# Performance work log

Hardware: AMD Instinct MI355X
Metric: run time of the kernel (lower is better)

## Reference

```python
import math
import jax, jax.numpy as jnp
import numpy as np

B, T, C, H = 1, 2048, 1024, 16


def _rope(q, k):
    # q, k: (B, H, T, D); interleaved RoPE exactly as the torch helper
    D = q.shape[-1]
    pos = jnp.arange(q.shape[2], dtype=jnp.float32)[:, None]           # (T, 1)
    div = jnp.exp(jnp.arange(0, D, 2, dtype=jnp.float32) * (-math.log(10000.0) / D))
    ang = pos * div                                                     # (T, D/2)
    sin = jnp.repeat(jnp.sin(ang), 2, axis=-1)                          # [s0,s0,s1,s1,...]
    cos = jnp.repeat(jnp.cos(ang), 2, axis=-1)

    def rot(x):
        x_alt = jnp.stack([-x[..., 1::2], x[..., ::2]], axis=-1).reshape(x.shape)
        return x * cos + x_alt * sin

    return rot(q), rot(k)


def setup_inputs() -> dict:
    key = jax.random.key(0)
    ks = jax.random.split(key, 5)
    s = 1.0 / math.sqrt(C)
    return {
        "x": jax.random.normal(ks[0], (B, T, C), dtype=jnp.float32),
        "Wq": jax.random.normal(ks[1], (C, C), dtype=jnp.float32) * s,
        "bq": jnp.zeros((C,), dtype=jnp.float32),
        "Wk": jax.random.normal(ks[2], (C, C), dtype=jnp.float32) * s,
        "bk": jnp.zeros((C,), dtype=jnp.float32),
        "Wv": jax.random.normal(ks[3], (C, C), dtype=jnp.float32) * s,
        "bv": jnp.zeros((C,), dtype=jnp.float32),
        "Wp": jax.random.normal(ks[4], (C, C), dtype=jnp.float32) * s,
        "bp": jnp.zeros((C,), dtype=jnp.float32),
    }


def reference(x, Wq, bq, Wk, bk, Wv, bv, Wp, bp):
    b, t, c = x.shape
    d = c // H
    # QKV projections -> (B, H, T, D)
    def split_heads(y):
        return y.reshape(b, t, H, d).transpose(0, 2, 1, 3)

    q = split_heads(x @ Wq + bq)
    k = split_heads(x @ Wk + bk)
    v = split_heads(x @ Wv + bv)
    q, k = _rope(q, k)

    scale = 1.0 / math.sqrt(d)
    att = jnp.einsum("bhqd,bhkd->bhqk", q, k) * scale                   # (B,H,T,T)
    causal = jnp.tril(jnp.ones((t, t), dtype=bool))                     # (T,T)
    att = jnp.where(causal[None, None], att, -jnp.inf)
    att = jax.nn.softmax(att, axis=-1)
    attn_save = att
    # dropout p=0 (eval) -> identity
    y = jnp.einsum("bhqk,bhkd->bhqd", att, v)                           # (B,H,T,D)
    y = y.transpose(0, 2, 1, 3).reshape(b, t, c)
    y = y @ Wp + bp
    return y, attn_save
```

## Files before the change

kernel.cpp:

```cpp
#include <hip/hip_runtime.h>

typedef unsigned short ushort_t;
typedef __bf16 bf16x8 __attribute__((ext_vector_type(8)));
typedef float f32x4 __attribute__((ext_vector_type(4)));

#define T_DIM 2048
#define C_DIM 1024
#define H_NUM 16
#define D_DIM 64

__device__ __forceinline__ ushort_t f2bf(float f){
  unsigned v = __float_as_uint(f);
  return (ushort_t)((v + 0x7fffu + ((v >> 16) & 1u)) >> 16);
}
__device__ __forceinline__ float bf2f(ushort_t u){
  return __uint_as_float(((unsigned)u) << 16);
}

typedef __attribute__((address_space(1))) const unsigned int* gas1_t;
typedef __attribute__((address_space(3))) unsigned int* las3_t;

__device__ __forceinline__ void gload_lds16(const void* g, void* l){
  __builtin_amdgcn_global_load_lds((gas1_t)g, (las3_t)l, 16, 0, 0);
}

__global__ __launch_bounds__(256) void prep_kernel(
    const float* __restrict__ x, ushort_t* __restrict__ xb,
    const float* __restrict__ w0, const float* __restrict__ w1,
    const float* __restrict__ w2, const float* __restrict__ w3,
    ushort_t* __restrict__ t0, ushort_t* __restrict__ t1,
    ushort_t* __restrict__ t2, ushort_t* __restrict__ t3)
{
  __shared__ float tl[64][65];
  const int bid = blockIdx.x;
  const int tid = threadIdx.x;
  if (bid >= 1024){
    int i = ((bid - 1024) * 256 + tid) * 4;
    float4 v = *reinterpret_cast<const float4*>(x + i);
    ushort4 o;
    o.x = f2bf(v.x); o.y = f2bf(v.y); o.z = f2bf(v.z); o.w = f2bf(v.w);
    *reinterpret_cast<ushort4*>(xb + i) = o;
    return;
  }
  const int which = bid >> 8;
  const float* W = which==0 ? w0 : which==1 ? w1 : which==2 ? w2 : w3;
  ushort_t* WT   = which==0 ? t0 : which==1 ? t1 : which==2 ? t2 : t3;
  const int tile = bid & 255;
  const int k0 = (tile & 15) * 64;
  const int n0 = (tile >> 4) * 64;
#pragma unroll
  for (int i = 0; i < 16; ++i){
    int idx = tid + i * 256;
    int r = idx >> 6, c = idx & 63;
    tl[r][c] = W[(k0 + r) * C_DIM + n0 + c];
  }
  __syncthreads();
#pragma unroll
  for (int i = 0; i < 16; ++i){
    int idx = tid + i * 256;
    int r = idx >> 6, c = idx & 63;
    WT[(n0 + r) * C_DIM + k0 + c] = f2bf(tl[c][r]);
  }
}

template<int MODE>
__global__ __launch_bounds__(256) void gemm_kernel(
    const ushort_t* __restrict__ A,
    const ushort_t* __restrict__ bt0, const ushort_t* __restrict__ bt1, const ushort_t* __restrict__ bt2,
    const float* __restrict__ bias0, const float* __restrict__ bias1, const float* __restrict__ bias2,
    ushort_t* __restrict__ o0, ushort_t* __restrict__ o1, ushort_t* __restrict__ o2,
    float* __restrict__ fo)
{
  __shared__ __align__(16) ushort_t Alds[64 * 32];
  __shared__ __align__(16) ushort_t Blds[128 * 32];
  const int tid = threadIdx.x;
  const int l15 = tid & 15, g = (tid & 63) >> 4;
  const int w = tid >> 6, wr = w >> 1, wc = w & 1;
  const int m0 = blockIdx.x * 64;
  int byy = blockIdx.y;
  int sel = 0;
  const ushort_t* BT; const float* bias; ushort_t* outp;
  if (MODE == 0){
    sel = byy >> 3; byy &= 7;
    BT   = sel==0 ? bt0 : (sel==1 ? bt1 : bt2);
    bias = sel==0 ? bias0 : (sel==1 ? bias1 : bias2);
    outp = sel==0 ? o0 : (sel==1 ? o1 : o2);
  } else { BT = bt0; bias = bias0; outp = o0; }
  const int n0 = byy * 128;

  const int c0 = tid, c1 = tid + 256;
  const ushort_t* Asrc  = A + (m0 + (c0 >> 2)) * C_DIM + (c0 & 3) * 8;
  const ushort_t* Bsrc0 = BT + (n0 + (c0 >> 2)) * C_DIM + (c0 & 3) * 8;
  const ushort_t* Bsrc1 = BT + (n0 + (c1 >> 2)) * C_DIM + (c1 & 3) * 8;

  f32x4 acc[2][4] = {};

  for (int kt = 0; kt < 32; ++kt){
    const int ko = kt * 32;
    gload_lds16(Asrc + ko, &Alds[c0 * 8]);
    gload_lds16(Bsrc0 + ko, &Blds[c0 * 8]);
    gload_lds16(Bsrc1 + ko, &Blds[c1 * 8]);
    __syncthreads();
    bf16x8 af[2], bfr[4];
#pragma unroll
    for (int i = 0; i < 2; ++i)
      af[i] = *reinterpret_cast<const bf16x8*>(&Alds[(wr * 32 + i * 16 + l15) * 32 + g * 8]);
#pragma unroll
    for (int j = 0; j < 4; ++j)
      bfr[j] = *reinterpret_cast<const bf16x8*>(&Blds[(wc * 64 + j * 16 + l15) * 32 + g * 8]);
#pragma unroll
    for (int i = 0; i < 2; ++i)
#pragma unroll
      for (int j = 0; j < 4; ++j)
        acc[i][j] = __builtin_amdgcn_mfma_f32_16x16x32_bf16(af[i], bfr[j], acc[i][j], 0, 0, 0);
    __syncthreads();
  }

  float bvv[4];
#pragma unroll
  for (int j = 0; j < 4; ++j) bvv[j] = bias[n0 + wc * 64 + j * 16 + l15];

  if (MODE == 1){
#pragma unroll
    for (int i = 0; i < 2; ++i)
#pragma unroll
      for (int j = 0; j < 4; ++j)
#pragma unroll
        for (int e = 0; e < 4; ++e){
          int t = m0 + wr * 32 + i * 16 + g * 4 + e;
          int c = n0 + wc * 64 + j * 16 + l15;
          fo[t * C_DIM + c] = acc[i][j][e] + bvv[j];
        }
    return;
  }

  if (sel == 2){
#pragma unroll
    for (int i = 0; i < 2; ++i){
#pragma unroll
      for (int j = 0; j < 4; ++j){
        int c = n0 + wc * 64 + j * 16 + l15;
        int hh = c >> 6, d = c & 63;
        int t0e = m0 + wr * 32 + i * 16 + g * 4;
        ushort4 o;
        o.x = f2bf(acc[i][j][0] + bvv[j]);
        o.y = f2bf(acc[i][j][1] + bvv[j]);
        o.z = f2bf(acc[i][j][2] + bvv[j]);
        o.w = f2bf(acc[i][j][3] + bvv[j]);
        *reinterpret_cast<ushort4*>(outp + (size_t)(hh * D_DIM + d) * T_DIM + t0e) = o;
      }
    }
  } else {
#pragma unroll
    for (int i = 0; i < 2; ++i){
#pragma unroll
      for (int j = 0; j < 4; ++j){
#pragma unroll
        for (int e = 0; e < 4; ++e){
          int t = m0 + wr * 32 + i * 16 + g * 4 + e;
          int c = n0 + wc * 64 + j * 16 + l15;
          int hh = c >> 6, d = c & 63;
          outp[((size_t)(hh * T_DIM) + t) * D_DIM + d] = f2bf(acc[i][j][e] + bvv[j]);
        }
      }
    }
  }
}

__global__ void rope_kernel(ushort_t* __restrict__ Qb, ushort_t* __restrict__ Kb){
  int gid = blockIdx.x * 256 + threadIdx.x;
  int which = gid >> 20;
  int r = gid & ((1 << 20) - 1);
  int i = r & 31;
  int t = (r >> 5) & 2047;
  int hh = r >> 16;
  ushort_t* P = which ? Kb : Qb;
  unsigned* p = reinterpret_cast<unsigned*>(P + ((hh * T_DIM) + t) * D_DIM + 2 * i);
  unsigned pv = *p;
  float x0 = bf2f((ushort_t)(pv & 0xffffu));
  float x1 = bf2f((ushort_t)(pv >> 16));
  float ang = (float)t * __expf((float)i * -0.2878231366242558f);
  float sn, cs;
  __sincosf(ang, &sn, &cs);
  float y0 = x0 * cs - x1 * sn;
  float y1 = x1 * cs + x0 * sn;
  *p = (unsigned)f2bf(y0) | (((unsigned)f2bf(y1)) << 16);
}

__global__ __launch_bounds__(256) void attn_kernel(
    const ushort_t* __restrict__ Qb, const ushort_t* __restrict__ Kb,
    const ushort_t* __restrict__ Vt, float* __restrict__ att, ushort_t* __restrict__ ya)
{
  __shared__ __align__(16) ushort_t Plds[2][64 * 72];
  __shared__ float m_sh[64], l_sh[64];

  const int tid = threadIdx.x;
  const int l15 = tid & 15, g = (tid & 63) >> 4;
  const int w = tid >> 6, wr = w >> 1, wc = w & 1;
  const int lin = (int)blockIdx.x;
  const int h = 2 * (lin & 7) + ((lin >> 3) & 1);
  const int qi = (T_DIM / 64 - 1) - (lin >> 4);
  const int q0 = qi * 64;
  const int nkt = qi + 1;

  const ushort_t* Qh = Qb + h * T_DIM * D_DIM;
  const ushort_t* Kh = Kb + h * T_DIM * D_DIM;
  const ushort_t* Vh = Vt + h * D_DIM * T_DIM;
  float* atth = att + (size_t)h * T_DIM * T_DIM;

  const f32x4 fz = {0.f, 0.f, 0.f, 0.f};
  const float scale = 0.125f;

  const int qloc = w * 16 + l15;
  const int qglob = q0 + qloc;
  bf16x8 qT[2];
#pragma unroll
  for (int ks = 0; ks < 2; ++ks)
    qT[ks] = *reinterpret_cast<const bf16x8*>(Qh + qglob * D_DIM + ks * 32 + g * 8);

  float m1 = -1e30f, l1 = 0.f;

  for (int kt = 0; kt < nkt; ++kt){
    f32x4 sc[4];
    sc[0] = fz; sc[1] = fz; sc[2] = fz; sc[3] = fz;
#pragma unroll
    for (int mblk = 0; mblk < 4; ++mblk){
#pragma unroll
      for (int ks = 0; ks < 2; ++ks){
        bf16x8 kfT = *reinterpret_cast<const bf16x8*>(
            Kh + (kt * 64 + mblk * 16 + l15) * D_DIM + ks * 32 + g * 8);
        sc[mblk] = __builtin_amdgcn_mfma_f32_16x16x32_bf16(kfT, qT[ks], sc[mblk], 0, 0, 0);
      }
    }
    const bool diag = (kt == qi);
    const int kbase = kt * 64 + g * 4;
    float sv[16];
    float mx = -1e30f;
#pragma unroll
    for (int mblk = 0; mblk < 4; ++mblk){
#pragma unroll
      for (int j = 0; j < 4; ++j){
        float s = sc[mblk][j] * scale;
        if (diag && (kbase + mblk * 16 + j) > qglob) s = -1e30f;
        sv[mblk * 4 + j] = s;
        mx = fmaxf(mx, s);
      }
    }
    mx = fmaxf(mx, __shfl_xor(mx, 16));
    mx = fmaxf(mx, __shfl_xor(mx, 32));
    float mn = fmaxf(m1, mx);
    float ps = 0.f;
#pragma unroll
    for (int i = 0; i < 16; ++i) ps += __expf(sv[i] - mn);
    ps += __shfl_xor(ps, 16);
    ps += __shfl_xor(ps, 32);
    l1 = l1 * __expf(m1 - mn) + ps;
    m1 = mn;
  }

  if ((tid & 48) == 0){ m_sh[qloc] = m1; l_sh[qloc] = l1; }
  __syncthreads();

  float Mrow[2][4], Li[2][4];
#pragma unroll
  for (int ms = 0; ms < 2; ++ms)
#pragma unroll
    for (int j = 0; j < 4; ++j){
      int row = wr * 32 + ms * 16 + g * 4 + j;
      Mrow[ms][j] = m_sh[row];
      Li[ms][j] = 1.0f / l_sh[row];
    }

  bf16x8 qf[2][2];
#pragma unroll
  for (int ms = 0; ms < 2; ++ms)
#pragma unroll
    for (int ks = 0; ks < 2; ++ks)
      qf[ms][ks] = *reinterpret_cast<const bf16x8*>(
          Qh + (q0 + wr * 32 + ms * 16 + l15) * D_DIM + ks * 32 + g * 8);

  f32x4 yac[2][2];
  yac[0][0] = fz; yac[0][1] = fz; yac[1][0] = fz; yac[1][1] = fz;

  int pb = 0;
  for (int kt = 0; kt < nkt; ++kt){
    ushort_t* Pb = &Plds[pb][0];
    bf16x8 kf[2][2];
#pragma unroll
    for (int ns = 0; ns < 2; ++ns)
#pragma unroll
      for (int ks = 0; ks < 2; ++ks)
        kf[ns][ks] = *reinterpret_cast<const bf16x8*>(
            Kh + (kt * 64 + wc * 32 + ns * 16 + l15) * D_DIM + ks * 32 + g * 8);

    f32x4 sac[2][2];
    sac[0][0] = fz; sac[0][1] = fz; sac[1][0] = fz; sac[1][1] = fz;
#pragma unroll
    for (int ms = 0; ms < 2; ++ms)
#pragma unroll
      for (int ns = 0; ns < 2; ++ns)
#pragma unroll
        for (int ks = 0; ks < 2; ++ks)
          sac[ms][ns] = __builtin_amdgcn_mfma_f32_16x16x32_bf16(qf[ms][ks], kf[ns][ks], sac[ms][ns], 0, 0, 0);

    const bool diag = (kt == qi);
#pragma unroll
    for (int ms = 0; ms < 2; ++ms)
#pragma unroll
      for (int ns = 0; ns < 2; ++ns)
#pragma unroll
        for (int j = 0; j < 4; ++j){
          float s = sac[ms][ns][j] * scale;
          int qq = wr * 32 + ms * 16 + g * 4 + j;
          int cc = wc * 32 + ns * 16 + l15;
          if (diag && cc > qq) s = -1e30f;
          float p = __expf(s - Mrow[ms][j]) * Li[ms][j];
          Pb[qq * 72 + cc] = f2bf(p);
        }
    __syncthreads();

    bf16x8 pf[2][2], vf[2][2];
#pragma unroll
    for (int ms = 0; ms < 2; ++ms)
#pragma unroll
      for (int kk = 0; kk < 2; ++kk)
        pf[ms][kk] = *reinterpret_cast<const bf16x8*>(
            &Pb[(wr * 32 + ms * 16 + l15) * 72 + kk * 32 + g * 8]);
#pragma unroll
    for (int nd = 0; nd < 2; ++nd)
#pragma unroll
      for (int kk = 0; kk < 2; ++kk)
        vf[nd][kk] = *reinterpret_cast<const bf16x8*>(
            Vh + (wc * 32 + nd * 16 + l15) * T_DIM + kt * 64 + kk * 32 + g * 8);
#pragma unroll
    for (int ms = 0; ms < 2; ++ms)
#pragma unroll
      for (int nd = 0; nd < 2; ++nd)
#pragma unroll
        for (int kk = 0; kk < 2; ++kk)
          yac[ms][nd] = __builtin_amdgcn_mfma_f32_16x16x32_bf16(pf[ms][kk], vf[nd][kk], yac[ms][nd], 0, 0, 0);

#pragma unroll
    for (int half = 0; half < 2; ++half){
      const int c = tid + half * 256;
      const int r = c >> 3, s = c & 7;
      union { int4 i4; ushort_t us[8]; } u;
      u.i4 = *reinterpret_cast<const int4*>(&Pb[r * 72 + s * 8]);
      f32x4 lo = { bf2f(u.us[0]), bf2f(u.us[1]), bf2f(u.us[2]), bf2f(u.us[3]) };
      f32x4 hi = { bf2f(u.us[4]), bf2f(u.us[5]), bf2f(u.us[6]), bf2f(u.us[7]) };
      float* dst = atth + (size_t)(q0 + r) * T_DIM + kt * 64 + s * 8;
      *reinterpret_cast<f32x4*>(dst)     = lo;
      *reinterpret_cast<f32x4*>(dst + 4) = hi;
    }
    pb ^= 1;
  }

  const int zc0 = nkt * 64;
  const int cpr = (T_DIM - zc0) >> 2;
  if (cpr > 0){
    const f32x4 z = {0.f, 0.f, 0.f, 0.f};
    for (int r = 0; r < 64; ++r){
      f32x4* dst = reinterpret_cast<f32x4*>(atth + (size_t)(q0 + r) * T_DIM + zc0);
      for (int i = tid; i < cpr; i += 256)
        dst[i] = z;
    }
  }

#pragma unroll
  for (int ms = 0; ms < 2; ++ms)
#pragma unroll
    for (int nd = 0; nd < 2; ++nd)
#pragma unroll
      for (int j = 0; j < 4; ++j){
        int t = q0 + wr * 32 + ms * 16 + g * 4 + j;
        int dcol = wc * 32 + nd * 16 + l15;
        ya[t * C_DIM + h * D_DIM + dcol] = f2bf(yac[ms][nd][j]);
      }
}

extern "C" void kernel_launch(void* const* d_in, const int* in_sizes, int n_in,
                              void* d_out, int out_size, void* d_ws, size_t ws_size,
                              hipStream_t stream)
{
  const float* x  = (const float*)d_in[0];
  const float* Wq = (const float*)d_in[1];
  const float* bq = (const float*)d_in[2];
  const float* Wk = (const float*)d_in[3];
  const float* bk = (const float*)d_in[4];
  const float* Wv = (const float*)d_in[5];
  const float* bv = (const float*)d_in[6];
  const float* Wp = (const float*)d_in[7];
  const float* bp = (const float*)d_in[8];
  float* out = (float*)d_out;
  char* ws = (char*)d_ws;

  ushort_t* xb  = (ushort_t*)(ws);
  ushort_t* wtq = (ushort_t*)(ws + (4u  << 20));
  ushort_t* wtk = (ushort_t*)(ws + (6u  << 20));
  ushort_t* wtv = (ushort_t*)(ws + (8u  << 20));
  ushort_t* wtp = (ushort_t*)(ws + (10u << 20));
  ushort_t* Qb  = (ushort_t*)(ws + (12u << 20));
  ushort_t* Kb  = (ushort_t*)(ws + (16u << 20));
  ushort_t* Vt  = (ushort_t*)(ws + (20u << 20));
  ushort_t* ya  = (ushort_t*)(ws + (24u << 20));

  hipLaunchKernelGGL(prep_kernel, dim3(3072), dim3(256), 0, stream,
                     x, xb, Wq, Wk, Wv, Wp, wtq, wtk, wtv, wtp);
  hipLaunchKernelGGL((gemm_kernel<0>), dim3(32, 24), dim3(256), 0, stream,
                     xb, wtq, wtk, wtv, bq, bk, bv, Qb, Kb, Vt, nullptr);
  hipLaunchKernelGGL(rope_kernel, dim3(8192), dim3(256), 0, stream, Qb, Kb);
  hipLaunchKernelGGL(attn_kernel, dim3(512), dim3(256), 0, stream,
                     Qb, Kb, Vt, out + 2097152, ya);
  hipLaunchKernelGGL((gemm_kernel<1>), dim3(32, 8), dim3(256), 0, stream,
                     ya, wtp, nullptr, nullptr, bp, nullptr, nullptr,
                     nullptr, nullptr, nullptr, out);
}
```

Before: 179.2 us.

## Split attention second pass across waves by key tiles with staged wide stores

Restructures the second attention pass so that each of the four waves processes a different key tile for the same 16-row query group, instead of splitting work in a 2x2 grid within one tile. Probabilities for up to 16 key tiles go into a wide LDS buffer, which is then written out to the attention matrix as a row-contiguous burst. Per-wave partial outputs are summed through LDS before the bf16 store. This removes the per-tile barrier and aims for longer contiguous writes to the large attention output. In exchange it adds a cross-wave reduction, reloads K and V fragments per row group, and leaves waves unevenly loaded on short causal rows.

```diff
diff --git a/kernel.cpp b/kernel.cpp
--- a/kernel.cpp
+++ b/kernel.cpp
@@ -8,6 +8,7 @@
 #define C_DIM 1024
 #define H_NUM 16
 #define D_DIM 64
+#define PWPAD 1032
 
 __device__ __forceinline__ ushort_t f2bf(float f){
   unsigned v = __float_as_uint(f);
@@ -191,12 +192,13 @@
     const ushort_t* __restrict__ Qb, const ushort_t* __restrict__ Kb,
     const ushort_t* __restrict__ Vt, float* __restrict__ att, ushort_t* __restrict__ ya)
 {
-  __shared__ __align__(16) ushort_t Plds[2][64 * 72];
+  __shared__ __align__(16) ushort_t Pw[16][PWPAD];
+  __shared__ __align__(16) float Osc[4][16][64];
   __shared__ float m_sh[64], l_sh[64];
 
   const int tid = threadIdx.x;
   const int l15 = tid & 15, g = (tid & 63) >> 4;
-  const int w = tid >> 6, wr = w >> 1, wc = w & 1;
+  const int w = tid >> 6;
   const int lin = (int)blockIdx.x;
   const int h = 2 * (lin & 7) + ((lin >> 3) & 1);
   const int qi = (T_DIM / 64 - 1) - (lin >> 4);
@@ -261,121 +263,112 @@
   if ((tid & 48) == 0){ m_sh[qloc] = m1; l_sh[qloc] = l1; }
   __syncthreads();
 
-  float Mrow[2][4], Li[2][4];
-#pragma unroll
-  for (int ms = 0; ms < 2; ++ms)
+  for (int rg = 0; rg < 4; ++rg){
+    bf16x8 qa[2];
+#pragma unroll
+    for (int ks = 0; ks < 2; ++ks)
+      qa[ks] = *reinterpret_cast<const bf16x8*>(
+          Qh + (q0 + rg * 16 + l15) * D_DIM + ks * 32 + g * 8);
+
+    float Mr[4], Lr[4];
 #pragma unroll
     for (int j = 0; j < 4; ++j){
-      int row = wr * 32 + ms * 16 + g * 4 + j;
-      Mrow[ms][j] = m_sh[row];
-      Li[ms][j] = 1.0f / l_sh[row];
-    }
-
-  bf16x8 qf[2][2];
-#pragma unroll
-  for (int ms = 0; ms < 2; ++ms)
-#pragma unroll
-    for (int ks = 0; ks < 2; ++ks)
-      qf[ms][ks] = *reinterpret_cast<const bf16x8*>(
-          Qh + (q0 + wr * 32 + ms * 16 + l15) * D_DIM + ks * 32 + g * 8);
-
-  f32x4 yac[2][2];
-  yac[0][0] = fz; yac[0][1] = fz; yac[1][0] = fz; yac[1][1] = fz;
-
-  int pb = 0;
-  for (int kt = 0; kt < nkt; ++kt){
-    ushort_t* Pb = &Plds[pb][0];
-    bf16x8 kf[2][2];
-#pragma unroll
-    for (int ns = 0; ns < 2; ++ns)
-#pragma unroll
-      for (int ks = 0; ks < 2; ++ks)
-        kf[ns][ks] = *reinterpret_cast<const bf16x8*>(
-            Kh + (kt * 64 + wc * 32 + ns * 16 + l15) * D_DIM + ks * 32 + g * 8);
-
-    f32x4 sac[2][2];
-    sac[0][0] = fz; sac[0][1] = fz; sac[1][0] = fz; sac[1][1] = fz;
-#pragma unroll
-    for (int ms = 0; ms < 2; ++ms)
-#pragma unroll
-      for (int ns = 0; ns < 2; ++ns)
-#pragma unroll
-        for (int ks = 0; ks < 2; ++ks)
-          sac[ms][ns] = __builtin_amdgcn_mfma_f32_16x16x32_bf16(qf[ms][ks], kf[ns][ks], sac[ms][ns], 0, 0, 0);
-
-    const bool diag = (kt == qi);
-#pragma unroll
-    for (int ms = 0; ms < 2; ++ms)
-#pragma unroll
-      for (int ns = 0; ns < 2; ++ns)
-#pragma unroll
-        for (int j = 0; j < 4; ++j){
-          float s = sac[ms][ns][j] * scale;
-          int qq = wr * 32 + ms * 16 + g * 4 + j;
-          int cc = wc * 32 + ns * 16 + l15;
-          if (diag && cc > qq) s = -1e30f;
-          float p = __expf(s - Mrow[ms][j]) * Li[ms][j];
-          Pb[qq * 72 + cc] = f2bf(p);
-        }
+      int row = rg * 16 + g * 4 + j;
+      Mr[j] = m_sh[row];
+      Lr[j] = 1.0f / l_sh[row];
+    }
+
+    f32x4 yac[4];
+    yac[0] = fz; yac[1] = fz; yac[2] = fz; yac[3] = fz;
+
+    const int nch = (nkt + 15) >> 4;
+    for (int ch = 0; ch < nch; ++ch){
+      const int ktbase = ch * 16;
+      const int ktend  = (ktbase + 16 < nkt) ? (ktbase + 16) : nkt;
+
+      for (int kt = ktbase + w; kt < ktend; kt += 4){
+        const int ktl = kt - ktbase;
+        f32x4 sac[4];
+        sac[0] = fz; sac[1] = fz; sac[2] = fz; sac[3] = fz;
+#pragma unroll
+        for (int ns = 0; ns < 4; ++ns){
+#pragma unroll
+          for (int ks = 0; ks < 2; ++ks){
+            bf16x8 kf = *reinterpret_cast<const bf16x8*>(
+                Kh + (kt * 64 + ns * 16 + l15) * D_DIM + ks * 32 + g * 8);
+            sac[ns] = __builtin_amdgcn_mfma_f32_16x16x32_bf16(qa[ks], kf, sac[ns], 0, 0, 0);
+          }
+        }
+        const bool diag = (kt == qi);
+#pragma unroll
+        for (int ns = 0; ns < 4; ++ns){
+#pragma unroll
+          for (int j = 0; j < 4; ++j){
+            float s = sac[ns][j] * scale;
+            int key = kt * 64 + ns * 16 + l15;
+            int qrow = q0 + rg * 16 + g * 4 + j;
+            if (diag && key > qrow) s = -1e30f;
+            float p = __expf(s - Mr[j]) * Lr[j];
+            Pw[g * 4 + j][ktl * 64 + ns * 16 + l15] = f2bf(p);
+          }
+        }
+#pragma unroll
+        for (int kk = 0; kk < 2; ++kk){
+          bf16x8 pf = *reinterpret_cast<const bf16x8*>(
+              &Pw[l15][ktl * 64 + kk * 32 + g * 8]);
+#pragma unroll
+          for (int nd = 0; nd < 4; ++nd){
+            bf16x8 vf = *reinterpret_cast<const bf16x8*>(
+                Vh + (nd * 16 + l15) * T_DIM + kt * 64 + kk * 32 + g * 8);
+            yac[nd] = __builtin_amdgcn_mfma_f32_16x16x32_bf16(pf, vf, yac[nd], 0, 0, 0);
+          }
+        }
+      }
+      __syncthreads();
+
+      const int wcols = (ktend - ktbase) * 64;
+      const int col = tid * 4;
+      if (col < wcols){
+#pragma unroll 4
+        for (int r = 0; r < 16; ++r){
+          ushort4 pv4 = *reinterpret_cast<const ushort4*>(&Pw[r][col]);
+          f32x4 o = { bf2f(pv4.x), bf2f(pv4.y), bf2f(pv4.z), bf2f(pv4.w) };
+          *reinterpret_cast<f32x4*>(
+              atth + (size_t)(q0 + rg * 16 + r) * T_DIM + ktbase * 64 + col) = o;
+        }
+      }
+      __syncthreads();
+    }
+
+    {
+      const int zc0 = nkt * 64;
+      for (int r = 0; r < 16; ++r){
+        float* rowp = atth + (size_t)(q0 + rg * 16 + r) * T_DIM;
+        for (int col = zc0 + tid * 4; col < T_DIM; col += 1024)
+          *reinterpret_cast<f32x4*>(rowp + col) = fz;
+      }
+    }
+
+#pragma unroll
+    for (int nd = 0; nd < 4; ++nd)
+#pragma unroll
+      for (int j = 0; j < 4; ++j)
+        Osc[w][g * 4 + j][nd * 16 + l15] = yac[nd][j];
     __syncthreads();
-
-    bf16x8 pf[2][2], vf[2][2];
-#pragma unroll
-    for (int ms = 0; ms < 2; ++ms)
-#pragma unroll
-      for (int kk = 0; kk < 2; ++kk)
-        pf[ms][kk] = *reinterpret_cast<const bf16x8*>(
-            &Pb[(wr * 32 + ms * 16 + l15) * 72 + kk * 32 + g * 8]);
-#pragma unroll
-    for (int nd = 0; nd < 2; ++nd)
-#pragma unroll
-      for (int kk = 0; kk < 2; ++kk)
-        vf[nd][kk] = *reinterpret_cast<const bf16x8*>(
-            Vh + (wc * 32 + nd * 16 + l15) * T_DIM + kt * 64 + kk * 32 + g * 8);
-#pragma unroll
-    for (int ms = 0; ms < 2; ++ms)
-#pragma unroll
-      for (int nd = 0; nd < 2; ++nd)
-#pragma unroll
-        for (int kk = 0; kk < 2; ++kk)
-          yac[ms][nd] = __builtin_amdgcn_mfma_f32_16x16x32_bf16(pf[ms][kk], vf[nd][kk], yac[ms][nd], 0, 0, 0);
-
-#pragma unroll
-    for (int half = 0; half < 2; ++half){
-      const int c = tid + half * 256;
-      const int r = c >> 3, s = c & 7;
-      union { int4 i4; ushort_t us[8]; } u;
-      u.i4 = *reinterpret_cast<const int4*>(&Pb[r * 72 + s * 8]);
-      f32x4 lo = { bf2f(u.us[0]), bf2f(u.us[1]), bf2f(u.us[2]), bf2f(u.us[3]) };
-      f32x4 hi = { bf2f(u.us[4]), bf2f(u.us[5]), bf2f(u.us[6]), bf2f(u.us[7]) };
-      float* dst = atth + (size_t)(q0 + r) * T_DIM + kt * 64 + s * 8;
-      *reinterpret_cast<f32x4*>(dst)     = lo;
-      *reinterpret_cast<f32x4*>(dst + 4) = hi;
-    }
-    pb ^= 1;
-  }
-
-  const int zc0 = nkt * 64;
-  const int cpr = (T_DIM - zc0) >> 2;
-  if (cpr > 0){
-    const f32x4 z = {0.f, 0.f, 0.f, 0.f};
-    for (int r = 0; r < 64; ++r){
-      f32x4* dst = reinterpret_cast<f32x4*>(atth + (size_t)(q0 + r) * T_DIM + zc0);
-      for (int i = tid; i < cpr; i += 256)
-        dst[i] = z;
-    }
-  }
-
-#pragma unroll
-  for (int ms = 0; ms < 2; ++ms)
-#pragma unroll
-    for (int nd = 0; nd < 2; ++nd)
-#pragma unroll
-      for (int j = 0; j < 4; ++j){
-        int t = q0 + wr * 32 + ms * 16 + g * 4 + j;
-        int dcol = wc * 32 + nd * 16 + l15;
-        ya[t * C_DIM + h * D_DIM + dcol] = f2bf(yac[ms][nd][j]);
-      }
+    {
+      const int f = tid * 4;
+      const int row = f >> 6, d = f & 63;
+      ushort4 o;
+      float s0 = Osc[0][row][d]     + Osc[1][row][d]     + Osc[2][row][d]     + Osc[3][row][d];
+      float s1 = Osc[0][row][d + 1] + Osc[1][row][d + 1] + Osc[2][row][d + 1] + Osc[3][row][d + 1];
+      float s2 = Osc[0][row][d + 2] + Osc[1][row][d + 2] + Osc[2][row][d + 2] + Osc[3][row][d + 2];
+      float s3 = Osc[0][row][d + 3] + Osc[1][row][d + 3] + Osc[2][row][d + 3] + Osc[3][row][d + 3];
+      o.x = f2bf(s0); o.y = f2bf(s1); o.z = f2bf(s2); o.w = f2bf(s3);
+      *reinterpret_cast<ushort4*>(
+          ya + (size_t)(q0 + rg * 16 + row) * C_DIM + h * D_DIM + d) = o;
+    }
+    __syncthreads();
+  }
 }
 
 extern "C" void kernel_launch(void* const* d_in, const int* in_sizes, int n_in,
```

After: 220.5 us. 1.23x slower.
